# Kernel optimization log

Measured on AMD Instinct MI355X. Metric: run time of the kernel, lower is better.

## Reference

```python
import jax, jax.numpy as jnp
import numpy as np

N_NODES = 100000
N_EDGES = 1600000
D_IN = 256
N_HEADS = 4
D_OUT = 32
NEG_SLOPE = 0.2


def setup_inputs() -> dict:
    key = jax.random.key(0)
    k1, k2, k3, k4, k5, k6 = jax.random.split(key, 6)
    x = jax.random.normal(k1, (N_NODES, D_IN), dtype=jnp.float32)
    fc_w = jax.random.normal(k2, (N_HEADS * D_OUT, D_IN), dtype=jnp.float32) * (1.0 / np.sqrt(D_IN))
    attn_l = jax.random.normal(k3, (N_HEADS, D_OUT), dtype=jnp.float32) * 0.1
    attn_r = jax.random.normal(k4, (N_HEADS, D_OUT), dtype=jnp.float32) * 0.1
    src = jax.random.randint(k5, (N_EDGES,), 0, N_NODES, dtype=jnp.int64)
    dst = jax.random.randint(k6, (N_EDGES,), 0, N_NODES, dtype=jnp.int64)
    return {"x": x, "fc_w": fc_w, "attn_l": attn_l, "attn_r": attn_r, "src": src, "dst": dst}


def reference(x, fc_w, attn_l, attn_r, src, dst):
    N = x.shape[0]
    H, F = attn_l.shape
    # Linear projection: ft = fc(x) viewed as [N, H, F]
    ft = (x @ fc_w.T).reshape(N, H, F)
    # Per-node attention logits: el = <ft, a_l>, er = <ft, a_r>  -> [N, H]
    el = jnp.einsum("nhf,hf->nh", ft, attn_l)
    er = jnp.einsum("nhf,hf->nh", ft, attn_r)
    # Edge scores: e = leaky_relu(el[src] + er[dst])  -> [E, H]
    e = el[src] + er[dst]
    e = jnp.where(e > 0, e, NEG_SLOPE * e)
    # Segment (per-destination-node) softmax over incoming edges
    m = jax.ops.segment_max(e, dst, num_segments=N)  # [N, H]
    ex = jnp.exp(e - m[dst])                          # [E, H]
    denom = jax.ops.segment_sum(ex, dst, num_segments=N)  # [N, H]
    a = ex / denom[dst]                               # [E, H]
    # Weighted scatter-sum aggregation: out[n] = sum_{e: dst=n} a_e * ft[src_e]
    out = jax.ops.segment_sum(ft[src] * a[:, :, None], dst, num_segments=N)  # [N, H, F]
    return out
```

## Files before the change

### kernel.cpp

```cpp
#include <hip/hip_runtime.h>
#include <math.h>

#define N_NODES 100000
#define N_EDGES 1600000
#define D_IN 256
#define N_HEADS 4
#define D_OUT 32
#define D_HID 128
#define NEG_SLOPE 0.2f

#define BUCKET_SHIFT 8
#define BUCKET_NODES 256
#define NB ((N_NODES + BUCKET_NODES - 1) / BUCKET_NODES)
#define CAP 6144
#define TILE 2048
#define EPT 8
#define N_TILES ((N_EDGES + TILE - 1) / TILE)

typedef __attribute__((ext_vector_type(8))) short bf16x8;
typedef __attribute__((ext_vector_type(4))) float f32x4;

static __device__ __forceinline__ unsigned cvt2(float lo, float hi) {
  unsigned r;
  asm("v_cvt_pk_bf16_f32 %0, %1, %2" : "=v"(r) : "v"(lo), "v"(hi));
  return r;
}
static __device__ __forceinline__ float bfu_lo(unsigned u) {
  union { unsigned u; float f; } c; c.u = u << 16; return c.f;
}
static __device__ __forceinline__ float bfu_hi(unsigned u) {
  union { unsigned u; float f; } c; c.u = u & 0xFFFF0000u; return c.f;
}

__global__ __launch_bounds__(256) void k_wcvt(const float* __restrict__ w,
                                              unsigned short* __restrict__ wb) {
  int i = blockIdx.x * 256 + threadIdx.x;
  if (i < (D_HID * D_IN) / 4) {
    float4 v = ((const float4*)w)[i];
    ((uint2*)wb)[i] = make_uint2(cvt2(v.x, v.y), cvt2(v.z, v.w));
  }
}

__global__ __launch_bounds__(256) void k_gemm(const float* __restrict__ x,
                                              const unsigned short* __restrict__ wb,
                                              const float* __restrict__ al,
                                              const float* __restrict__ ar,
                                              unsigned short* __restrict__ ftb,
                                              float* __restrict__ el,
                                              float* __restrict__ er) {
  int t = threadIdx.x;
  int wave = t >> 6, lane = t & 63;
  int quad = lane >> 4, l16 = lane & 15;
  int rowBase = blockIdx.x * 256 + wave * 64;

  f32x4 acc[4][8];
  #pragma unroll
  for (int mt = 0; mt < 4; ++mt)
    #pragma unroll
    for (int nt = 0; nt < 8; ++nt) {
      acc[mt][nt][0] = 0.f; acc[mt][nt][1] = 0.f;
      acc[mt][nt][2] = 0.f; acc[mt][nt][3] = 0.f;
    }

  const float* xr[4];
  bool rv[4];
  #pragma unroll
  for (int mt = 0; mt < 4; ++mt) {
    int row = rowBase + mt * 16 + l16;
    rv[mt] = row < N_NODES;
    xr[mt] = x + (size_t)(rv[mt] ? row : 0) * D_IN + quad * 8;
  }
  const unsigned short* wr = wb + l16 * D_IN + quad * 8;
  const float4 z4 = make_float4(0.f, 0.f, 0.f, 0.f);

  float4 xb[4][2];
  #pragma unroll
  for (int mt = 0; mt < 4; ++mt) {
    xb[mt][0] = rv[mt] ? *(const float4*)(xr[mt]) : z4;
    xb[mt][1] = rv[mt] ? *(const float4*)(xr[mt] + 4) : z4;
  }

  #pragma unroll
  for (int kb = 0; kb < D_IN; kb += 32) {
    float4 xn[4][2];
    if (kb + 32 < D_IN) {
      #pragma unroll
      for (int mt = 0; mt < 4; ++mt) {
        xn[mt][0] = rv[mt] ? *(const float4*)(xr[mt] + kb + 32) : z4;
        xn[mt][1] = rv[mt] ? *(const float4*)(xr[mt] + kb + 36) : z4;
      }
    }
    bf16x8 bfr[8];
    #pragma unroll
    for (int nt = 0; nt < 8; ++nt)
      bfr[nt] = *(const bf16x8*)(wr + nt * 16 * D_IN + kb);
    bf16x8 af[4];
    #pragma unroll
    for (int mt = 0; mt < 4; ++mt) {
      union { unsigned u[4]; bf16x8 v; } c;
      c.u[0] = cvt2(xb[mt][0].x, xb[mt][0].y);
      c.u[1] = cvt2(xb[mt][0].z, xb[mt][0].w);
      c.u[2] = cvt2(xb[mt][1].x, xb[mt][1].y);
      c.u[3] = cvt2(xb[mt][1].z, xb[mt][1].w);
      af[mt] = c.v;
    }
    #pragma unroll
    for (int mt = 0; mt < 4; ++mt)
      #pragma unroll
      for (int nt = 0; nt < 8; ++nt)
        acc[mt][nt] = __builtin_amdgcn_mfma_f32_16x16x32_bf16(af[mt], bfr[nt], acc[mt][nt], 0, 0, 0);
    if (kb + 32 < D_IN) {
      #pragma unroll
      for (int mt = 0; mt < 4; ++mt) {
        xb[mt][0] = xn[mt][0];
        xb[mt][1] = xn[mt][1];
      }
    }
  }

  #pragma unroll
  for (int mt = 0; mt < 4; ++mt) {
    #pragma unroll
    for (int nt = 0; nt < 8; ++nt) {
      int col = nt * 16 + l16;
      #pragma unroll
      for (int r = 0; r < 4; r += 2) {
        unsigned p = cvt2(acc[mt][nt][r], acc[mt][nt][r + 1]);
        int row = rowBase + mt * 16 + quad * 4 + r;
        if (row < N_NODES)
          ftb[(size_t)row * D_HID + col] = (unsigned short)p;
        if (row + 1 < N_NODES)
          ftb[(size_t)(row + 1) * D_HID + col] = (unsigned short)(p >> 16);
      }
    }
  }

  float alf[8], arf[8];
  #pragma unroll
  for (int nt = 0; nt < 8; ++nt) {
    alf[nt] = al[nt * 16 + l16];
    arf[nt] = ar[nt * 16 + l16];
  }
  #pragma unroll
  for (int mt = 0; mt < 4; ++mt) {
    #pragma unroll
    for (int r = 0; r < 4; ++r) {
      int row = rowBase + mt * 16 + quad * 4 + r;
      float sl[4], sr[4];
      #pragma unroll
      for (int h = 0; h < 4; ++h) {
        sl[h] = acc[mt][2 * h][r] * alf[2 * h] + acc[mt][2 * h + 1][r] * alf[2 * h + 1];
        sr[h] = acc[mt][2 * h][r] * arf[2 * h] + acc[mt][2 * h + 1][r] * arf[2 * h + 1];
      }
      #pragma unroll
      for (int o = 1; o < 16; o <<= 1) {
        #pragma unroll
        for (int h = 0; h < 4; ++h) {
          sl[h] += __shfl_xor(sl[h], o);
          sr[h] += __shfl_xor(sr[h], o);
        }
      }
      if (l16 == 0 && row < N_NODES) {
        *(float4*)&el[row * 4] = make_float4(sl[0], sl[1], sl[2], sl[3]);
        *(float4*)&er[row * 4] = make_float4(sr[0], sr[1], sr[2], sr[3]);
      }
    }
  }
}

__global__ __launch_bounds__(256) void k_bucket(const int* __restrict__ src,
                                                const int* __restrict__ dst,
                                                int* __restrict__ gfill,
                                                unsigned* __restrict__ pairs,
                                                int* __restrict__ offs) {
  __shared__ int bcnt[NB];
  __shared__ int brsv[NB];
  __shared__ int brank[NB];
  int t = threadIdx.x;
  if (blockIdx.x == 0 && t == 0) offs[N_NODES] = N_EDGES;
  for (int tile = blockIdx.x; tile < N_TILES; tile += gridDim.x) {
    int e0 = tile * TILE + t * EPT;
    for (int i = t; i < NB; i += 256) { bcnt[i] = 0; brank[i] = 0; }
    __syncthreads();
    int ds[EPT], ss[EPT];
    if (e0 + EPT <= N_EDGES) {
      *(int4*)&ds[0] = *(const int4*)&dst[e0];
      *(int4*)&ds[4] = *(const int4*)&dst[e0 + 4];
      *(int4*)&ss[0] = *(const int4*)&src[e0];
      *(int4*)&ss[4] = *(const int4*)&src[e0 + 4];
    } else {
      #pragma unroll
      for (int k = 0; k < EPT; ++k) {
        int e = e0 + k;
        ds[k] = (e < N_EDGES) ? dst[e] : -1;
        ss[k] = (e < N_EDGES) ? src[e] : 0;
      }
    }
    #pragma unroll
    for (int k = 0; k < EPT; ++k)
      if (ds[k] >= 0) atomicAdd(&bcnt[ds[k] >> BUCKET_SHIFT], 1);
    __syncthreads();
    for (int i = t; i < NB; i += 256) {
      int c = bcnt[i];
      brsv[i] = (c > 0) ? atomicAdd(&gfill[i], c) : 0;
    }
    __syncthreads();
    #pragma unroll
    for (int k = 0; k < EPT; ++k) {
      if (ds[k] >= 0) {
        int b = ds[k] >> BUCKET_SHIFT;
        int r = brsv[b] + atomicAdd(&brank[b], 1);
        if (r < CAP)
          pairs[(size_t)b * CAP + r] =
              ((unsigned)ss[k] << 8) | (unsigned)(ds[k] & (BUCKET_NODES - 1));
      }
    }
    __syncthreads();
  }
}

__global__ __launch_bounds__(512) void k_localsort(const unsigned* __restrict__ pairs,
                                                   const int* __restrict__ gfill,
                                                   int* __restrict__ offs,
                                                   int* __restrict__ ssrc) {
  __shared__ int cnt_l[256];
  __shared__ int ss[256];
  __shared__ int cur_l[256];
  __shared__ int redsum[8];
  __shared__ int s_base;
  int b = blockIdx.x, t = threadIdx.x;
  {
    int v = (t < NB && t < b) ? gfill[t] : 0;
    #pragma unroll
    for (int o = 32; o > 0; o >>= 1) v += __shfl_xor(v, o);
    if ((t & 63) == 0) redsum[t >> 6] = v;
  }
  if (t < 256) cnt_l[t] = 0;
  __syncthreads();
  if (t == 0) {
    int s = 0;
    #pragma unroll
    for (int i = 0; i < 8; ++i) s += redsum[i];
    s_base = s;
  }
  int E = min(gfill[b], CAP);
  const unsigned* pb = &pairs[(size_t)b * CAP];
  __syncthreads();
  int base = s_base;
  for (int i = t; i < E; i += 512)
    atomicAdd(&cnt_l[pb[i] & (BUCKET_NODES - 1)], 1);
  __syncthreads();
  if (t < 256) ss[t] = cnt_l[t];
  __syncthreads();
  #pragma unroll
  for (int d = 1; d < 256; d <<= 1) {
    int u = (t < 256 && t >= d) ? ss[t - d] : 0;
    __syncthreads();
    if (t < 256) ss[t] += u;
    __syncthreads();
  }
  if (t < 256) {
    int pre = (t == 0) ? 0 : ss[t - 1];
    int node = b * BUCKET_NODES + t;
    if (node < N_NODES) offs[node] = base + pre;
    cur_l[t] = pre;
  }
  __syncthreads();
  for (int i = t; i < E; i += 512) {
    unsigned p = pb[i];
    int pos = atomicAdd(&cur_l[p & (BUCKET_NODES - 1)], 1);
    ssrc[base + pos] = (int)(p >> 8);
  }
}

#define AH_PAD 36
__global__ __launch_bounds__(256) void k_agg(const int* __restrict__ offs,
                                             const int* __restrict__ ssrc,
                                             const unsigned short* __restrict__ ftb,
                                             const float* __restrict__ el,
                                             const float* __restrict__ er,
                                             float* __restrict__ out) {
  __shared__ int   lds_s[4][2][32];
  __shared__ float lds_ah[4][2][4][AH_PAD];
  int wave = threadIdx.x >> 6;
  int lane = threadIdx.x & 63;
  int half = lane >> 5;
  int l32 = lane & 31;
  int n = blockIdx.x * 8 + wave * 2 + half;
  if (n >= N_NODES) return;
  int start = offs[n], end = offs[n + 1];
  int deg = end - start;

  int* sS = lds_s[wave][half];
  float (*sA)[AH_PAD] = lds_ah[wave][half];

  int c4 = l32 * 4;
  int hh = l32 >> 3;
  const unsigned short* fb = ftb + c4;
  float a0 = 0.f, a1 = 0.f, a2 = 0.f, a3 = 0.f;

  float4 er4 = *(const float4*)&er[n * 4];

  if (deg <= 32) {
    bool valid = l32 < deg;
    int s = valid ? ssrc[start + l32] : 0;
    float4 e4 = *(const float4*)&el[s * 4];
    float v[4] = {e4.x + er4.x, e4.y + er4.y, e4.z + er4.z, e4.w + er4.w};
    float m[4], ex[4], den[4];
    #pragma unroll
    for (int h = 0; h < 4; ++h) {
      v[h] = v[h] > 0.f ? v[h] : NEG_SLOPE * v[h];
      m[h] = valid ? v[h] : -INFINITY;
    }
    #pragma unroll
    for (int h = 0; h < 4; ++h)
      #pragma unroll
      for (int o = 16; o > 0; o >>= 1) m[h] = fmaxf(m[h], __shfl_xor(m[h], o));
    #pragma unroll
    for (int h = 0; h < 4; ++h) {
      ex[h] = valid ? __expf(v[h] - m[h]) : 0.f;
      den[h] = ex[h];
    }
    #pragma unroll
    for (int h = 0; h < 4; ++h)
      #pragma unroll
      for (int o = 16; o > 0; o >>= 1) den[h] += __shfl_xor(den[h], o);
    sS[l32] = s;
    #pragma unroll
    for (int h = 0; h < 4; ++h) sA[h][l32] = ex[h] / den[h];
    __builtin_amdgcn_wave_barrier();
    for (int j = 0; j < deg; j += 4) {
      int4   sv = *(const int4*)&sS[j];
      float4 av = *(const float4*)&sA[hh][j];
      uint2 uA = *(const uint2*)&fb[(size_t)sv.x * D_HID];
      uint2 uB = *(const uint2*)&fb[(size_t)sv.y * D_HID];
      uint2 uC = *(const uint2*)&fb[(size_t)sv.z * D_HID];
      uint2 uD = *(const uint2*)&fb[(size_t)sv.w * D_HID];
      a0 += av.x * bfu_lo(uA.x); a1 += av.x * bfu_hi(uA.x);
      a2 += av.x * bfu_lo(uA.y); a3 += av.x * bfu_hi(uA.y);
      a0 += av.y * bfu_lo(uB.x); a1 += av.y * bfu_hi(uB.x);
      a2 += av.y * bfu_lo(uB.y); a3 += av.y * bfu_hi(uB.y);
      a0 += av.z * bfu_lo(uC.x); a1 += av.z * bfu_hi(uC.x);
      a2 += av.z * bfu_lo(uC.y); a3 += av.z * bfu_hi(uC.y);
      a0 += av.w * bfu_lo(uD.x); a1 += av.w * bfu_hi(uD.x);
      a2 += av.w * bfu_lo(uD.y); a3 += av.w * bfu_hi(uD.y);
    }
  } else {
    float erh[4] = {er4.x, er4.y, er4.z, er4.w};
    float m[4] = {-INFINITY, -INFINITY, -INFINITY, -INFINITY};
    for (int c = start; c < end; c += 32) {
      int i = c + l32;
      bool valid = i < end;
      int s = valid ? ssrc[i] : 0;
      float4 e4 = *(const float4*)&el[s * 4];
      float ee[4] = {e4.x, e4.y, e4.z, e4.w};
      #pragma unroll
      for (int h = 0; h < 4; ++h) {
        float v = ee[h] + erh[h];
        v = v > 0.f ? v : NEG_SLOPE * v;
        m[h] = fmaxf(m[h], valid ? v : -INFINITY);
      }
    }
    #pragma unroll
    for (int h = 0; h < 4; ++h)
      #pragma unroll
      for (int o = 16; o > 0; o >>= 1) m[h] = fmaxf(m[h], __shfl_xor(m[h], o));
    float den[4] = {0.f, 0.f, 0.f, 0.f};
    for (int c = start; c < end; c += 32) {
      int i = c + l32;
      bool valid = i < end;
      int s = valid ? ssrc[i] : 0;
      float4 e4 = *(const float4*)&el[s * 4];
      float ee[4] = {e4.x, e4.y, e4.z, e4.w};
      #pragma unroll
      for (int h = 0; h < 4; ++h) {
        float v = ee[h] + erh[h];
        v = v > 0.f ? v : NEG_SLOPE * v;
        den[h] += valid ? __expf(v - m[h]) : 0.f;
      }
    }
    #pragma unroll
    for (int h = 0; h < 4; ++h)
      #pragma unroll
      for (int o = 16; o > 0; o >>= 1) den[h] += __shfl_xor(den[h], o);
    float invd[4];
    #pragma unroll
    for (int h = 0; h < 4; ++h) invd[h] = 1.f / den[h];
    for (int c = start; c < end; c += 32) {
      int i = c + l32;
      bool valid = i < end;
      int s = valid ? ssrc[i] : 0;
      float4 e4 = *(const float4*)&el[s * 4];
      float ee[4] = {e4.x, e4.y, e4.z, e4.w};
      float av[4];
      #pragma unroll
      for (int h = 0; h < 4; ++h) {
        float v = ee[h] + erh[h];
        v = v > 0.f ? v : NEG_SLOPE * v;
        av[h] = valid ? __expf(v - m[h]) * invd[h] : 0.f;
      }
      __builtin_amdgcn_wave_barrier();
      sS[l32] = s;
      #pragma unroll
      for (int h = 0; h < 4; ++h) sA[h][l32] = av[h];
      __builtin_amdgcn_wave_barrier();
      int cnt = min(32, end - c);
      for (int j = 0; j < cnt; j += 4) {
        int4   sv = *(const int4*)&sS[j];
        float4 aw = *(const float4*)&sA[hh][j];
        uint2 uA = *(const uint2*)&fb[(size_t)sv.x * D_HID];
        uint2 uB = *(const uint2*)&fb[(size_t)sv.y * D_HID];
        uint2 uC = *(const uint2*)&fb[(size_t)sv.z * D_HID];
        uint2 uD = *(const uint2*)&fb[(size_t)sv.w * D_HID];
        a0 += aw.x * bfu_lo(uA.x); a1 += aw.x * bfu_hi(uA.x);
        a2 += aw.x * bfu_lo(uA.y); a3 += aw.x * bfu_hi(uA.y);
        a0 += aw.y * bfu_lo(uB.x); a1 += aw.y * bfu_hi(uB.x);
        a2 += aw.y * bfu_lo(uB.y); a3 += aw.y * bfu_hi(uB.y);
        a0 += aw.z * bfu_lo(uC.x); a1 += aw.z * bfu_hi(uC.x);
        a2 += aw.z * bfu_lo(uC.y); a3 += aw.z * bfu_hi(uC.y);
        a0 += aw.w * bfu_lo(uD.x); a1 += aw.w * bfu_hi(uD.x);
        a2 += aw.w * bfu_lo(uD.y); a3 += aw.w * bfu_hi(uD.y);
      }
    }
  }
  *(float4*)&out[(size_t)n * D_HID + c4] = make_float4(a0, a1, a2, a3);
}

extern "C" void kernel_launch(void* const* d_in, const int* in_sizes, int n_in,
                              void* d_out, int out_size, void* d_ws, size_t ws_size,
                              hipStream_t stream) {
  const float* x      = (const float*)d_in[0];
  const float* fc_w   = (const float*)d_in[1];
  const float* attn_l = (const float*)d_in[2];
  const float* attn_r = (const float*)d_in[3];
  const int*   src    = (const int*)d_in[4];
  const int*   dst    = (const int*)d_in[5];
  float* out = (float*)d_out;

  char* wsp = (char*)d_ws;
  size_t off = 0;
  auto alloc = [&](size_t bytes) {
    void* p = wsp + off;
    off = (off + bytes + 255) & ~(size_t)255;
    return p;
  };
  unsigned short* ftb = (unsigned short*)alloc((size_t)N_NODES * D_HID * 2);
  unsigned short* wb  = (unsigned short*)alloc((size_t)D_HID * D_IN * 2);
  float* el     = (float*)alloc((size_t)N_NODES * 4 * 4);
  float* er     = (float*)alloc((size_t)N_NODES * 4 * 4);
  int*   offs   = (int*)alloc((size_t)(N_NODES + 1) * 4);
  int*   ssrc   = (int*)alloc((size_t)N_EDGES * 4);
  int*   gfill  = (int*)alloc((size_t)NB * 4);
  unsigned* pairs = (unsigned*)alloc((size_t)NB * CAP * 4);

  hipMemsetAsync(gfill, 0, (size_t)NB * 4, stream);
  k_wcvt<<<(D_HID * D_IN / 4 + 255) / 256, 256, 0, stream>>>(fc_w, wb);
  k_gemm<<<(N_NODES + 255) / 256, 256, 0, stream>>>(x, wb, attn_l, attn_r, ftb, el, er);
  k_bucket<<<N_TILES, 256, 0, stream>>>(src, dst, gfill, pairs, offs);
  k_localsort<<<NB, 512, 0, stream>>>(pairs, gfill, offs, ssrc);
  k_agg<<<(N_NODES + 7) / 8, 256, 0, stream>>>(offs, ssrc, ftb, el, er, out);
}
```

Before: 351.8 us.

## Stage GEMM A and W tiles in swizzled LDS with 128-row blocks

The projection GEMM now has each block cooperatively load its 128 input rows (converted to bf16) and the full bf16 weight matrix into 128 KB of XOR-swizzled shared memory. MFMA operands are then read from LDS instead of every wave fetching weights and x fragments from global memory with strided loads. Rows per block drop from 256 to 128 and the grid doubles, with occupancy pinned to one block per CU. The large LDS footprint limits latency hiding, there is no overlap between loads and compute, and the weight matrix is reloaded by every block.

```diff
diff --git a/kernel.cpp b/kernel.cpp
--- a/kernel.cpp
+++ b/kernel.cpp
@@ -41,85 +41,74 @@
   }
 }
 
-__global__ __launch_bounds__(256) void k_gemm(const float* __restrict__ x,
-                                              const unsigned short* __restrict__ wb,
-                                              const float* __restrict__ al,
-                                              const float* __restrict__ ar,
-                                              unsigned short* __restrict__ ftb,
-                                              float* __restrict__ el,
-                                              float* __restrict__ er) {
+__global__ __launch_bounds__(256, 1) void k_gemm(const float* __restrict__ x,
+                                                 const unsigned short* __restrict__ wb,
+                                                 const float* __restrict__ al,
+                                                 const float* __restrict__ ar,
+                                                 unsigned short* __restrict__ ftb,
+                                                 float* __restrict__ el,
+                                                 float* __restrict__ er) {
+  __shared__ char lds[131072];
+  char* As = lds;
+  char* Ws = lds + 65536;
   int t = threadIdx.x;
   int wave = t >> 6, lane = t & 63;
   int quad = lane >> 4, l16 = lane & 15;
-  int rowBase = blockIdx.x * 256 + wave * 64;
-
-  f32x4 acc[4][8];
-  #pragma unroll
-  for (int mt = 0; mt < 4; ++mt)
+  int rowBlk = blockIdx.x * 128;
+
+  {
+    int r = t >> 1, h = t & 1;
+    int grow = rowBlk + r;
+    bool v = grow < N_NODES;
+    const float* xp = x + (size_t)(v ? grow : 0) * D_IN + h * 128;
+    unsigned swz = (unsigned)((r & 7) << 4);
+    char* abase = As + r * 512 + h * 256;
+    char* wbase = Ws + r * 512 + h * 256;
+    const uint4* wp = (const uint4*)wb + t * 16;
+    const float4 z4 = make_float4(0.f, 0.f, 0.f, 0.f);
+    #pragma unroll
+    for (int c = 0; c < 16; ++c) {
+      float4 v0 = v ? *(const float4*)(xp + c * 8) : z4;
+      float4 v1 = v ? *(const float4*)(xp + c * 8 + 4) : z4;
+      uint4 wv = wp[c];
+      uint4 av = make_uint4(cvt2(v0.x, v0.y), cvt2(v0.z, v0.w),
+                            cvt2(v1.x, v1.y), cvt2(v1.z, v1.w));
+      *(uint4*)(abase + ((unsigned)(c * 16) ^ swz)) = av;
+      *(uint4*)(wbase + ((unsigned)(c * 16) ^ swz)) = wv;
+    }
+  }
+  __syncthreads();
+
+  f32x4 acc[2][8];
+  #pragma unroll
+  for (int mt = 0; mt < 2; ++mt)
     #pragma unroll
     for (int nt = 0; nt < 8; ++nt) {
       acc[mt][nt][0] = 0.f; acc[mt][nt][1] = 0.f;
       acc[mt][nt][2] = 0.f; acc[mt][nt][3] = 0.f;
     }
-
-  const float* xr[4];
-  bool rv[4];
-  #pragma unroll
-  for (int mt = 0; mt < 4; ++mt) {
-    int row = rowBase + mt * 16 + l16;
-    rv[mt] = row < N_NODES;
-    xr[mt] = x + (size_t)(rv[mt] ? row : 0) * D_IN + quad * 8;
-  }
-  const unsigned short* wr = wb + l16 * D_IN + quad * 8;
-  const float4 z4 = make_float4(0.f, 0.f, 0.f, 0.f);
-
-  float4 xb[4][2];
-  #pragma unroll
-  for (int mt = 0; mt < 4; ++mt) {
-    xb[mt][0] = rv[mt] ? *(const float4*)(xr[mt]) : z4;
-    xb[mt][1] = rv[mt] ? *(const float4*)(xr[mt] + 4) : z4;
-  }
-
-  #pragma unroll
-  for (int kb = 0; kb < D_IN; kb += 32) {
-    float4 xn[4][2];
-    if (kb + 32 < D_IN) {
-      #pragma unroll
-      for (int mt = 0; mt < 4; ++mt) {
-        xn[mt][0] = rv[mt] ? *(const float4*)(xr[mt] + kb + 32) : z4;
-        xn[mt][1] = rv[mt] ? *(const float4*)(xr[mt] + kb + 36) : z4;
-      }
-    }
-    bf16x8 bfr[8];
+  unsigned swzL = (unsigned)((l16 & 7) << 4);
+  int m0 = wave * 32 + l16;
+  #pragma unroll
+  for (int kb = 0; kb < 8; ++kb) {
+    unsigned ko = (unsigned)(kb * 64 + quad * 16);
+    bf16x8 a0 = *(const bf16x8*)(As + m0 * 512 + (ko ^ swzL));
+    bf16x8 a1 = *(const bf16x8*)(As + (m0 + 16) * 512 + (ko ^ swzL));
+    bf16x8 b[8];
     #pragma unroll
     for (int nt = 0; nt < 8; ++nt)
-      bfr[nt] = *(const bf16x8*)(wr + nt * 16 * D_IN + kb);
-    bf16x8 af[4];
-    #pragma unroll
-    for (int mt = 0; mt < 4; ++mt) {
-      union { unsigned u[4]; bf16x8 v; } c;
-      c.u[0] = cvt2(xb[mt][0].x, xb[mt][0].y);
-      c.u[1] = cvt2(xb[mt][0].z, xb[mt][0].w);
-      c.u[2] = cvt2(xb[mt][1].x, xb[mt][1].y);
-      c.u[3] = cvt2(xb[mt][1].z, xb[mt][1].w);
-      af[mt] = c.v;
-    }
-    #pragma unroll
-    for (int mt = 0; mt < 4; ++mt)
-      #pragma unroll
-      for (int nt = 0; nt < 8; ++nt)
-        acc[mt][nt] = __builtin_amdgcn_mfma_f32_16x16x32_bf16(af[mt], bfr[nt], acc[mt][nt], 0, 0, 0);
-    if (kb + 32 < D_IN) {
-      #pragma unroll
-      for (int mt = 0; mt < 4; ++mt) {
-        xb[mt][0] = xn[mt][0];
-        xb[mt][1] = xn[mt][1];
-      }
-    }
-  }
-
-  #pragma unroll
-  for (int mt = 0; mt < 4; ++mt) {
+      b[nt] = *(const bf16x8*)(Ws + (nt * 16 + l16) * 512 + (ko ^ swzL));
+    #pragma unroll
+    for (int nt = 0; nt < 8; ++nt) {
+      acc[0][nt] = __builtin_amdgcn_mfma_f32_16x16x32_bf16(a0, b[nt], acc[0][nt], 0, 0, 0);
+      acc[1][nt] = __builtin_amdgcn_mfma_f32_16x16x32_bf16(a1, b[nt], acc[1][nt], 0, 0, 0);
+    }
+  }
+
+  int rowBase = rowBlk + wave * 32;
+
+  #pragma unroll
+  for (int mt = 0; mt < 2; ++mt) {
     #pragma unroll
     for (int nt = 0; nt < 8; ++nt) {
       int col = nt * 16 + l16;
@@ -142,7 +131,7 @@
     arf[nt] = ar[nt * 16 + l16];
   }
   #pragma unroll
-  for (int mt = 0; mt < 4; ++mt) {
+  for (int mt = 0; mt < 2; ++mt) {
     #pragma unroll
     for (int r = 0; r < 4; ++r) {
       int row = rowBase + mt * 16 + quad * 4 + r;
@@ -455,7 +444,7 @@
 
   hipMemsetAsync(gfill, 0, (size_t)NB * 4, stream);
   k_wcvt<<<(D_HID * D_IN / 4 + 255) / 256, 256, 0, stream>>>(fc_w, wb);
-  k_gemm<<<(N_NODES + 255) / 256, 256, 0, stream>>>(x, wb, attn_l, attn_r, ftb, el, er);
+  k_gemm<<<(N_NODES + 127) / 128, 256, 0, stream>>>(x, wb, attn_l, attn_r, ftb, el, er);
   k_bucket<<<N_TILES, 256, 0, stream>>>(src, dst, gfill, pairs, offs);
   k_localsort<<<NB, 512, 0, stream>>>(pairs, gfill, offs, ssrc);
   k_agg<<<(N_NODES + 7) / 8, 256, 0, stream>>>(offs, ssrc, ftb, el, er, out);
```

Measured after the change: 366.3 us. 1.04x slower.
